# Kernel tuning notes

Measured on AMD Instinct MI355X. Metric: run time of the kernel, lower is better.

## Reference

```python
import jax, jax.numpy as jnp
import numpy as np

N_NODES = 50000
N_EDGES = 800000
IN_DIM = 128
HID = 32
HEADS = 4
OUT_DIM = 2
NEG_SLOPE = 0.2


def gat_conv(feat, W, al, ar, bias, src, dst, n_nodes):
    """DGL GATConv (eval mode, no dropout). feat: [N, Fin]; W: [Fin, H*D];
    al, ar: [H, D]; bias: [H*D]. Returns [N, H, D]."""
    H, D = al.shape
    hf = (feat @ W).reshape(n_nodes, H, D)              # [N,H,D]
    el = jnp.einsum('nhd,hd->nh', hf, al)               # [N,H]
    er = jnp.einsum('nhd,hd->nh', hf, ar)               # [N,H]
    e = el[src] + er[dst]                               # [E,H]
    e = jax.nn.leaky_relu(e, NEG_SLOPE)
    # segment softmax over incoming edges of each dst node
    emax = jax.ops.segment_max(e, dst, num_segments=n_nodes)  # [N,H]
    emax = jnp.where(jnp.isfinite(emax), emax, 0.0)
    ex = jnp.exp(e - emax[dst])                         # [E,H]
    denom = jax.ops.segment_sum(ex, dst, num_segments=n_nodes)  # [N,H]
    alpha = ex / jnp.maximum(denom[dst], 1e-30)         # [E,H]
    msg = hf[src] * alpha[:, :, None]                   # [E,H,D]
    out = jax.ops.segment_sum(msg, dst, num_segments=n_nodes)   # [N,H,D]
    return out + bias.reshape(1, H, D)


def setup_inputs() -> dict:
    key = jax.random.key(0)
    ks = jax.random.split(key, 16)
    f32 = jnp.float32
    in_feat = jax.random.normal(ks[0], (N_NODES, IN_DIM), dtype=f32)
    src = jax.random.randint(ks[1], (N_EDGES,), 0, N_NODES)
    dst = jax.random.randint(ks[2], (N_EDGES,), 0, N_NODES)
    s1 = 1.0 / np.sqrt(IN_DIM)
    s2 = 1.0 / np.sqrt(HID * HEADS)
    W1 = jax.random.normal(ks[3], (IN_DIM, HEADS * HID), dtype=f32) * s1
    al1 = jax.random.normal(ks[4], (HEADS, HID), dtype=f32) * 0.1
    ar1 = jax.random.normal(ks[5], (HEADS, HID), dtype=f32) * 0.1
    b1 = jnp.zeros((HEADS * HID,), dtype=f32)
    W2 = jax.random.normal(ks[6], (HEADS * HID, HEADS * HID), dtype=f32) * s2
    al2 = jax.random.normal(ks[7], (HEADS, HID), dtype=f32) * 0.1
    ar2 = jax.random.normal(ks[8], (HEADS, HID), dtype=f32) * 0.1
    b2 = jnp.zeros((HEADS * HID,), dtype=f32)
    Wout = jax.random.normal(ks[9], (HID, OUT_DIM), dtype=f32) * (1.0 / np.sqrt(HID))
    bout = jnp.zeros((OUT_DIM,), dtype=f32)
    return {"in_feat": in_feat, "W1": W1, "al1": al1, "ar1": ar1, "b1": b1,
            "W2": W2, "al2": al2, "ar2": ar2, "b2": b2,
            "Wout": Wout, "bout": bout, "src": src, "dst": dst}


def reference(in_feat, W1, al1, ar1, b1, W2, al2, ar2, b2, Wout, bout, src, dst):
    h = gat_conv(in_feat, W1, al1, ar1, b1, src, dst, N_NODES)  # [N,H,D]
    h = jax.nn.relu(h.reshape(N_NODES, HEADS * HID))            # flatten(1) + relu
    h = gat_conv(h, W2, al2, ar2, b2, src, dst, N_NODES)        # [N,H,D]
    emd = h.mean(axis=1)                                        # mean over heads -> [N,D]
    logits = jax.nn.relu(emd) @ Wout + bout                     # [N,2]
    return jax.nn.softmax(logits, axis=-1)
```

## Files before the change

kernel.cpp:

```cpp
#include <hip/hip_runtime.h>
#include <cmath>

#define N_NODES 50000
#define N_EDGES 800000
#define NBUCK 196
#define NHB 196
#define EPB 4096

typedef unsigned short u16;
typedef unsigned int u32;
typedef __attribute__((ext_vector_type(8))) short bf16x8;
typedef __attribute__((ext_vector_type(4))) float f32x4;

static __device__ __forceinline__ float lrelu(float x) { return x > 0.f ? x : 0.2f * x; }
static __device__ __forceinline__ float bf2f(u16 u) { return __uint_as_float(((u32)u) << 16); }
static __device__ __forceinline__ u16 f2bf(float f) {
    u32 b = __float_as_uint(f);
    return (u16)((b + 0x7FFFu + ((b >> 16) & 1u)) >> 16);
}
static __device__ __forceinline__ u32 pack2(float a, float b) {
    return (u32)f2bf(a) | ((u32)f2bf(b) << 16);
}
static __device__ __forceinline__ float sx(u32 u, int k) {
    return (float)((int)(u << ((3 - k) * 8)) >> 24);
}

__global__ __launch_bounds__(1024) void bhist_pack_k(const int* __restrict__ dst, u32* __restrict__ bcnt,
                                                     const float* __restrict__ W1, const float* __restrict__ W2,
                                                     u16* __restrict__ Wp1, u16* __restrict__ Wp2,
                                                     u32* __restrict__ done) {
    int tid = threadIdx.x;
    if (blockIdx.x < NHB) {
        __shared__ u32 hist[NBUCK];
        for (int i = tid; i < NBUCK; i += 1024) hist[i] = 0;
        __syncthreads();
        int base = blockIdx.x * EPB;
#pragma unroll
        for (int k = 0; k < 4; ++k) {
            int e = base + k * 1024 + tid;
            if (e < N_EDGES) atomicAdd(&hist[dst[e] >> 8], 1u);
        }
        __syncthreads();
        for (int i = tid; i < NBUCK; i += 1024) bcnt[(size_t)i * NHB + blockIdx.x] = hist[i];
    } else {
        if (blockIdx.x == NHB && tid == 0) *done = 0;
        int gi = (blockIdx.x - NHB) * 1024 + tid;
        const float* W = (gi < 16384) ? W1 : W2;
        u16* Wp = (gi < 16384) ? Wp1 : Wp2;
        int i = gi & 16383;
        int j = i & 7, lane = (i >> 3) & 63, ks = (i >> 9) & 3, nt = i >> 11;
        int k = ks * 32 + (lane >> 4) * 8 + j;
        int ncol = nt * 16 + (lane & 15);
        Wp[i] = f2bf(W[k * 128 + ncol]);
    }
}

__global__ __launch_bounds__(256) void scant_k(const u32* __restrict__ bcnt, u32* __restrict__ wbase,
                                               u32* __restrict__ btot, int* __restrict__ bstart,
                                               u32* __restrict__ done) {
    __shared__ u32 s[256];
    __shared__ bool amLast;
    int i = blockIdx.x, t = threadIdx.x;
    u32 v = (t < NHB) ? bcnt[(size_t)i * NHB + t] : 0;
    s[t] = v;
    __syncthreads();
    for (int o = 1; o < 256; o <<= 1) {
        u32 x = (t >= o) ? s[t - o] : 0;
        __syncthreads();
        s[t] += x;
        __syncthreads();
    }
    if (t < NHB) wbase[(size_t)i * NHB + t] = s[t] - v;
    if (t == 255) atomicExch(&btot[i], s[255]);
    __threadfence();
    if (t == 0) amLast = (atomicAdd(done, 1u) == NBUCK - 1);
    __syncthreads();
    if (!amLast) return;
    __threadfence();
    u32 v2 = (t < NBUCK) ? atomicAdd(&btot[t], 0u) : 0;
    s[t] = v2;
    __syncthreads();
    for (int o = 1; o < 256; o <<= 1) {
        u32 x = (t >= o) ? s[t - o] : 0;
        __syncthreads();
        s[t] += x;
        __syncthreads();
    }
    if (t < NBUCK) bstart[t] = (int)(s[t] - v2);
    if (t == NBUCK - 1) bstart[NBUCK] = (int)s[t];
}

__global__ __launch_bounds__(1024) void bscatter_k(const int* __restrict__ src, const int* __restrict__ dst,
                                                   const u32* __restrict__ wbase, const int* __restrict__ bstart,
                                                   u32* __restrict__ bucketed) {
    __shared__ u32 pos[NBUCK];
    int tid = threadIdx.x;
    for (int i = tid; i < NBUCK; i += 1024)
        pos[i] = (u32)bstart[i] + wbase[(size_t)i * NHB + blockIdx.x];
    __syncthreads();
    int base = blockIdx.x * EPB;
#pragma unroll
    for (int k = 0; k < 4; ++k) {
        int e = base + k * 1024 + tid;
        if (e < N_EDGES) {
            int d = dst[e];
            int b = d >> 8;
            u32 p = atomicAdd(&pos[b], 1u);
            bucketed[p] = (u32)src[e] | ((u32)(d & 255) << 16);
        }
    }
}

__global__ __launch_bounds__(1024) void bcsr_k(const u32* __restrict__ bucketed, const int* __restrict__ bstart,
                                               int* __restrict__ offs, u16* __restrict__ srcs) {
    __shared__ u32 cnt[256];
    __shared__ int s[256];
    __shared__ u32 fp[256];
    int b = blockIdx.x;
    int tid = threadIdx.x;
    int ebeg = bstart[b], eend = bstart[b + 1];
    int ne = eend - ebeg;
    if (tid < 256) cnt[tid] = 0;
    __syncthreads();
    for (int i = tid; i < ne; i += 1024)
        atomicAdd(&cnt[bucketed[ebeg + i] >> 16], 1u);
    __syncthreads();
    if (tid < 256) s[tid] = (int)cnt[tid];
    __syncthreads();
    for (int o = 1; o < 256; o <<= 1) {
        int v = (tid < 256 && tid >= o) ? s[tid - o] : 0;
        __syncthreads();
        if (tid < 256) s[tid] += v;
        __syncthreads();
    }
    if (tid < 256) {
        int excl = s[tid] - (int)cnt[tid];
        int node = b * 256 + tid;
        if (node < N_NODES) offs[node] = ebeg + excl;
        fp[tid] = (u32)excl;
    }
    if (b == NBUCK - 1 && tid == 0) offs[N_NODES] = N_EDGES;
    __syncthreads();
    for (int i = tid; i < ne; i += 1024) {
        u32 u = bucketed[ebeg + i];
        u32 p = atomicAdd(&fp[u >> 16], 1u);
        srcs[ebeg + p] = (u16)(u & 0xFFFFu);
    }
}

template <int BF16IN>
__global__ __launch_bounds__(256) void gemm_mfma(
    const void* __restrict__ Xv, const u16* __restrict__ Wp,
    const float* __restrict__ al, const float* __restrict__ ar,
    signed char* __restrict__ hq, float2* __restrict__ elhs, float* __restrict__ er, int n)
{
    __shared__ u16 xs[64][136];
    int row0 = blockIdx.x * 64;
    int tid = threadIdx.x;
    if (BF16IN) {
        const uint4* Xb = (const uint4*)Xv;
        for (int i = tid; i < 1024; i += 256) {
            int r = i >> 4, c = i & 15;
            uint4 v = make_uint4(0u, 0u, 0u, 0u);
            if (row0 + r < n) v = Xb[(size_t)(row0 + r) * 16 + c];
            ((uint4*)&xs[r][0])[c] = v;
        }
    } else {
        const float4* X4 = (const float4*)Xv;
        for (int i = tid; i < 2048; i += 256) {
            int r = i >> 5, c = i & 31;
            float4 v = make_float4(0.f, 0.f, 0.f, 0.f);
            if (row0 + r < n) v = X4[(size_t)(row0 + r) * 32 + c];
            ((uint2*)&xs[r][0])[c] = make_uint2(pack2(v.x, v.y), pack2(v.z, v.w));
        }
    }
    __syncthreads();

    int wave = tid >> 6, lane = tid & 63;
    int quad = lane >> 4, l15 = lane & 15;

    bf16x8 bfrag[2][4];
#pragma unroll
    for (int ct = 0; ct < 2; ++ct) {
        int nt = wave * 2 + ct;
#pragma unroll
        for (int ks = 0; ks < 4; ++ks)
            bfrag[ct][ks] = *(const bf16x8*)(Wp + ((((nt * 4 + ks) * 64) + lane) << 3));
    }

    f32x4 acc[4][2];
#pragma unroll
    for (int rt = 0; rt < 4; ++rt)
#pragma unroll
        for (int ct = 0; ct < 2; ++ct)
            acc[rt][ct] = (f32x4){0.f, 0.f, 0.f, 0.f};

#pragma unroll
    for (int ks = 0; ks < 4; ++ks) {
#pragma unroll
        for (int rt = 0; rt < 4; ++rt) {
            bf16x8 a = *(const bf16x8*)&xs[rt * 16 + l15][ks * 32 + quad * 8];
            acc[rt][0] = __builtin_amdgcn_mfma_f32_16x16x32_bf16(a, bfrag[0][ks], acc[rt][0], 0, 0, 0);
            acc[rt][1] = __builtin_amdgcn_mfma_f32_16x16x32_bf16(a, bfrag[1][ks], acc[rt][1], 0, 0, 0);
        }
    }

    float alv0 = al[wave * 32 + l15], alv1 = al[wave * 32 + 16 + l15];
    float arv0 = ar[wave * 32 + l15], arv1 = ar[wave * 32 + 16 + l15];
#pragma unroll
    for (int rt = 0; rt < 4; ++rt) {
#pragma unroll
        for (int r = 0; r < 4; ++r) {
            int row = row0 + rt * 16 + quad * 4 + r;
            float c0 = acc[rt][0][r], c1 = acc[rt][1][r];
            float m = fmaxf(fabsf(c0), fabsf(c1));
            m = fmaxf(m, __shfl_xor(m, 1));
            m = fmaxf(m, __shfl_xor(m, 2));
            m = fmaxf(m, __shfl_xor(m, 4));
            m = fmaxf(m, __shfl_xor(m, 8));
            m = fmaxf(m, 1e-20f);
            float qsc = 127.0f / m;
            if (row < n) {
                hq[(size_t)row * 128 + wave * 32 + l15] = (signed char)(int)rintf(c0 * qsc);
                hq[(size_t)row * 128 + wave * 32 + 16 + l15] = (signed char)(int)rintf(c1 * qsc);
            }
            float pel = c0 * alv0 + c1 * alv1;
            float per = c0 * arv0 + c1 * arv1;
            pel += __shfl_xor(pel, 1); pel += __shfl_xor(pel, 2);
            pel += __shfl_xor(pel, 4); pel += __shfl_xor(pel, 8);
            per += __shfl_xor(per, 1); per += __shfl_xor(per, 2);
            per += __shfl_xor(per, 4); per += __shfl_xor(per, 8);
            if (l15 == 0 && row < n) {
                elhs[row * 4 + wave] = make_float2(pel, m * (1.0f / 127.0f));
                er[row * 4 + wave] = per;
            }
        }
    }
}

static __device__ __forceinline__ void agg_core(
    int node, int lane, const int* __restrict__ offs, const u16* __restrict__ srcs,
    const float2* __restrict__ elhs, const float* __restrict__ er,
    const signed char* __restrict__ hq,
    float acc[8], float& den)
{
    int qw = lane >> 4;
    int q = lane & 15;
    int h = q >> 2;
    float erh = er[node * 4 + h];
    int beg = offs[node], end = offs[node + 1];
    int deg = end - beg;
    den = 0.f;
#pragma unroll
    for (int i = 0; i < 8; i++) acc[i] = 0.f;

    if (deg <= 64) {
        int psrc = (lane < deg) ? (int)srcs[beg + lane] : 0;
        int base = beg;
        for (; base + 16 <= end; base += 16) {
            int j = base - beg + qw;
            int ss[4];
            ss[0] = __shfl(psrc, j);
            ss[1] = __shfl(psrc, j + 4);
            ss[2] = __shfl(psrc, j + 8);
            ss[3] = __shfl(psrc, j + 12);
            float2 eh[4];
            uint2 uv[4];
#pragma unroll
            for (int k = 0; k < 4; ++k) {
                eh[k] = elhs[ss[k] * 4 + h];
                uv[k] = *(const uint2*)(hq + (size_t)ss[k] * 128 + q * 8);
            }
#pragma unroll
            for (int k = 0; k < 4; ++k) {
                float w = __expf(lrelu(eh[k].x + erh));
                float ws = w * eh[k].y;
                den += w;
                acc[0] += ws * sx(uv[k].x, 0);
                acc[1] += ws * sx(uv[k].x, 1);
                acc[2] += ws * sx(uv[k].x, 2);
                acc[3] += ws * sx(uv[k].x, 3);
                acc[4] += ws * sx(uv[k].y, 0);
                acc[5] += ws * sx(uv[k].y, 1);
                acc[6] += ws * sx(uv[k].y, 2);
                acc[7] += ws * sx(uv[k].y, 3);
            }
        }
        for (; base + 8 <= end; base += 8) {
            int j = base - beg + qw;
            int s0 = __shfl(psrc, j);
            int s1 = __shfl(psrc, j + 4);
            float2 e0 = elhs[s0 * 4 + h], e1 = elhs[s1 * 4 + h];
            uint2 u0 = *(const uint2*)(hq + (size_t)s0 * 128 + q * 8);
            uint2 u1 = *(const uint2*)(hq + (size_t)s1 * 128 + q * 8);
            float w0 = __expf(lrelu(e0.x + erh));
            float w1 = __expf(lrelu(e1.x + erh));
            float ws0 = w0 * e0.y, ws1 = w1 * e1.y;
            den += w0 + w1;
            acc[0] += ws0 * sx(u0.x, 0) + ws1 * sx(u1.x, 0);
            acc[1] += ws0 * sx(u0.x, 1) + ws1 * sx(u1.x, 1);
            acc[2] += ws0 * sx(u0.x, 2) + ws1 * sx(u1.x, 2);
            acc[3] += ws0 * sx(u0.x, 3) + ws1 * sx(u1.x, 3);
            acc[4] += ws0 * sx(u0.y, 0) + ws1 * sx(u1.y, 0);
            acc[5] += ws0 * sx(u0.y, 1) + ws1 * sx(u1.y, 1);
            acc[6] += ws0 * sx(u0.y, 2) + ws1 * sx(u1.y, 2);
            acc[7] += ws0 * sx(u0.y, 3) + ws1 * sx(u1.y, 3);
        }
        for (; base < end; base += 4) {
            int e = base + qw;
            bool valid = e < end;
            int j = valid ? (e - beg) : 0;
            int s = __shfl(psrc, j);
            float2 eh = elhs[s * 4 + h];
            float w = valid ? __expf(lrelu(eh.x + erh)) : 0.f;
            float ws = w * eh.y;
            uint2 u = *(const uint2*)(hq + (size_t)s * 128 + q * 8);
            den += w;
            acc[0] += ws * sx(u.x, 0);
            acc[1] += ws * sx(u.x, 1);
            acc[2] += ws * sx(u.x, 2);
            acc[3] += ws * sx(u.x, 3);
            acc[4] += ws * sx(u.y, 0);
            acc[5] += ws * sx(u.y, 1);
            acc[6] += ws * sx(u.y, 2);
            acc[7] += ws * sx(u.y, 3);
        }
    } else {
        for (int base = beg; base < end; base += 4) {
            int e = base + qw;
            bool valid = e < end;
            int ec = valid ? e : end - 1;
            int s = srcs[ec];
            float2 eh = elhs[s * 4 + h];
            float w = valid ? __expf(lrelu(eh.x + erh)) : 0.f;
            float ws = w * eh.y;
            uint2 u = *(const uint2*)(hq + (size_t)s * 128 + q * 8);
            den += w;
            acc[0] += ws * sx(u.x, 0);
            acc[1] += ws * sx(u.x, 1);
            acc[2] += ws * sx(u.x, 2);
            acc[3] += ws * sx(u.x, 3);
            acc[4] += ws * sx(u.y, 0);
            acc[5] += ws * sx(u.y, 1);
            acc[6] += ws * sx(u.y, 2);
            acc[7] += ws * sx(u.y, 3);
        }
    }
#pragma unroll
    for (int i = 0; i < 8; i++) {
        acc[i] += __shfl_xor(acc[i], 16);
        acc[i] += __shfl_xor(acc[i], 32);
    }
    den += __shfl_xor(den, 16);
    den += __shfl_xor(den, 32);
}

__global__ __launch_bounds__(256) void agg1_gemm2_k(
    const int* __restrict__ offs, const u16* __restrict__ srcs,
    const float2* __restrict__ elhs1, const float* __restrict__ er1,
    const signed char* __restrict__ hq1, const float* __restrict__ b1,
    const u16* __restrict__ Wp2, const float* __restrict__ al2, const float* __restrict__ ar2,
    signed char* __restrict__ hq2, float2* __restrict__ elhs2, float* __restrict__ er2)
{
    __shared__ u16 xs[16][136];
    int row0 = blockIdx.x * 16;
    int tid = threadIdx.x;
    int wave = tid >> 6, lane = tid & 63;
    int q = lane & 15;

    float bv[8];
#pragma unroll
    for (int i = 0; i < 8; i++) bv[i] = b1[q * 8 + i];

#pragma unroll
    for (int it = 0; it < 4; ++it) {
        int ln = wave * 4 + it;
        int node = row0 + ln;
        float acc[8], den;
        agg_core(node, lane, offs, srcs, elhs1, er1, hq1, acc, den);
        if (lane < 16) {
            float inv = 1.0f / fmaxf(den, 1e-30f);
            float o[8];
#pragma unroll
            for (int i = 0; i < 8; i++)
                o[i] = fmaxf(acc[i] * inv + bv[i], 0.f);
            uint4 pk;
            pk.x = pack2(o[0], o[1]);
            pk.y = pack2(o[2], o[3]);
            pk.z = pack2(o[4], o[5]);
            pk.w = pack2(o[6], o[7]);
            ((uint4*)&xs[ln][0])[q] = pk;
        }
    }
    __syncthreads();

    int quad = lane >> 4, l15 = lane & 15;

    bf16x8 bfrag[2][4];
#pragma unroll
    for (int ct = 0; ct < 2; ++ct) {
        int nt = wave * 2 + ct;
#pragma unroll
        for (int ks = 0; ks < 4; ++ks)
            bfrag[ct][ks] = *(const bf16x8*)(Wp2 + ((((nt * 4 + ks) * 64) + lane) << 3));
    }

    f32x4 acc2[2];
    acc2[0] = (f32x4){0.f, 0.f, 0.f, 0.f};
    acc2[1] = (f32x4){0.f, 0.f, 0.f, 0.f};

#pragma unroll
    for (int ks = 0; ks < 4; ++ks) {
        bf16x8 a = *(const bf16x8*)&xs[l15][ks * 32 + quad * 8];
        acc2[0] = __builtin_amdgcn_mfma_f32_16x16x32_bf16(a, bfrag[0][ks], acc2[0], 0, 0, 0);
        acc2[1] = __builtin_amdgcn_mfma_f32_16x16x32_bf16(a, bfrag[1][ks], acc2[1], 0, 0, 0);
    }

    float alv0 = al2[wave * 32 + l15], alv1 = al2[wave * 32 + 16 + l15];
    float arv0 = ar2[wave * 32 + l15], arv1 = ar2[wave * 32 + 16 + l15];
#pragma unroll
    for (int r = 0; r < 4; ++r) {
        int row = row0 + quad * 4 + r;
        float c0 = acc2[0][r], c1 = acc2[1][r];
        float m = fmaxf(fabsf(c0), fabsf(c1));
        m = fmaxf(m, __shfl_xor(m, 1));
        m = fmaxf(m, __shfl_xor(m, 2));
        m = fmaxf(m, __shfl_xor(m, 4));
        m = fmaxf(m, __shfl_xor(m, 8));
        m = fmaxf(m, 1e-20f);
        float qsc = 127.0f / m;
        hq2[(size_t)row * 128 + wave * 32 + l15] = (signed char)(int)rintf(c0 * qsc);
        hq2[(size_t)row * 128 + wave * 32 + 16 + l15] = (signed char)(int)rintf(c1 * qsc);
        float pel = c0 * alv0 + c1 * alv1;
        float per = c0 * arv0 + c1 * arv1;
        pel += __shfl_xor(pel, 1); pel += __shfl_xor(pel, 2);
        pel += __shfl_xor(pel, 4); pel += __shfl_xor(pel, 8);
        per += __shfl_xor(per, 1); per += __shfl_xor(per, 2);
        per += __shfl_xor(per, 4); per += __shfl_xor(per, 8);
        if (l15 == 0) {
            elhs2[row * 4 + wave] = make_float2(pel, m * (1.0f / 127.0f));
            er2[row * 4 + wave] = per;
        }
    }
}

__global__ __launch_bounds__(256) void agg2_k(const int* __restrict__ offs, const u16* __restrict__ srcs,
                                              const float2* __restrict__ elhs, const float* __restrict__ er,
                                              const signed char* __restrict__ hq,
                                              const float* __restrict__ bias,
                                              const float* __restrict__ Wout, const float* __restrict__ bout,
                                              float2* __restrict__ out) {
    int node = blockIdx.x * 4 + (threadIdx.x >> 6);
    int lane = threadIdx.x & 63;
    if (node >= N_NODES) return;
    float acc[8], den;
    agg_core(node, lane, offs, srcs, elhs, er, hq, acc, den);
    int q = lane & 15;
    float inv = 1.0f / fmaxf(den, 1e-30f);
    float o[8];
#pragma unroll
    for (int i = 0; i < 8; i++) o[i] = acc[i] * inv + bias[q * 8 + i];
#pragma unroll
    for (int i = 0; i < 8; i++) {
        o[i] += __shfl_xor(o[i], 4);
        o[i] += __shfl_xor(o[i], 8);
        o[i] = fmaxf(0.25f * o[i], 0.f);
    }
    int d0 = (q & 3) * 8;
    float l0 = 0.f, l1 = 0.f;
#pragma unroll
    for (int i = 0; i < 8; i++) {
        l0 += o[i] * Wout[(d0 + i) * 2];
        l1 += o[i] * Wout[(d0 + i) * 2 + 1];
    }
    l0 += __shfl_xor(l0, 1); l0 += __shfl_xor(l0, 2);
    l1 += __shfl_xor(l1, 1); l1 += __shfl_xor(l1, 2);
    if (lane == 0) {
        l0 += bout[0];
        l1 += bout[1];
        float mx = fmaxf(l0, l1);
        float e0 = __expf(l0 - mx), e1 = __expf(l1 - mx);
        float invs = 1.f / (e0 + e1);
        out[node] = make_float2(e0 * invs, e1 * invs);
    }
}

extern "C" void kernel_launch(void* const* d_in, const int* in_sizes, int n_in,
                              void* d_out, int out_size, void* d_ws, size_t ws_size,
                              hipStream_t stream) {
    const float* in_feat = (const float*)d_in[0];
    const float* W1   = (const float*)d_in[1];
    const float* al1  = (const float*)d_in[2];
    const float* ar1  = (const float*)d_in[3];
    const float* b1   = (const float*)d_in[4];
    const float* W2   = (const float*)d_in[5];
    const float* al2  = (const float*)d_in[6];
    const float* ar2  = (const float*)d_in[7];
    const float* b2   = (const float*)d_in[8];
    const float* Wout = (const float*)d_in[9];
    const float* bout = (const float*)d_in[10];
    const int*   src  = (const int*)d_in[11];
    const int*   dst  = (const int*)d_in[12];
    float* out = (float*)d_out;

    char* ws = (char*)d_ws;
    size_t off = 0;
    auto carve = [&](size_t bytes) {
        char* p = ws + off;
        off = (off + bytes + 255) & ~(size_t)255;
        return p;
    };
    signed char* hq  = (signed char*)carve((size_t)N_NODES * 128);
    float2* elhs     = (float2*)carve((size_t)N_NODES * 4 * 8);
    float* er        = (float*)carve((size_t)N_NODES * 4 * 4);
    signed char* hq2 = (signed char*)carve((size_t)N_NODES * 128);
    float2* elhs2    = (float2*)carve((size_t)N_NODES * 4 * 8);
    float* er2       = (float*)carve((size_t)N_NODES * 4 * 4);
    u16*   srcs      = (u16*)carve((size_t)N_EDGES * 2);
    u32*   bucketed  = (u32*)carve((size_t)N_EDGES * 4);
    u32*   bcnt      = (u32*)carve((size_t)NBUCK * NHB * 4);
    u32*   wbase     = (u32*)carve((size_t)NBUCK * NHB * 4);
    u32*   btot      = (u32*)carve((size_t)NBUCK * 4);
    int*   bstart    = (int*)carve((size_t)(NBUCK + 1) * 4);
    int*   offs      = (int*)carve((size_t)(N_NODES + 1) * 4);
    u16*   Wp1       = (u16*)carve((size_t)16384 * 2);
    u16*   Wp2       = (u16*)carve((size_t)16384 * 2);
    u32*   done      = (u32*)carve(256);
    (void)ws_size; (void)in_sizes; (void)n_in; (void)out_size;

    const int GB = (N_NODES + 63) / 64;
    const int FB = N_NODES / 16;
    const int AB = (N_NODES + 3) / 4;

    bhist_pack_k<<<NHB + 32, 1024, 0, stream>>>(dst, bcnt, W1, W2, Wp1, Wp2, done);
    scant_k<<<NBUCK, 256, 0, stream>>>(bcnt, wbase, btot, bstart, done);
    bscatter_k<<<NHB, 1024, 0, stream>>>(src, dst, wbase, bstart, bucketed);
    bcsr_k<<<NBUCK, 1024, 0, stream>>>(bucketed, bstart, offs, srcs);

    gemm_mfma<0><<<GB, 256, 0, stream>>>(in_feat, Wp1, al1, ar1, hq, elhs, er, N_NODES);

    agg1_gemm2_k<<<FB, 256, 0, stream>>>(offs, srcs, elhs, er, hq, b1, Wp2, al2, ar2, hq2, elhs2, er2);

    agg2_k<<<AB, 256, 0, stream>>>(offs, srcs, elhs2, er2, hq2, b2, Wout, bout, (float2*)out);
}
```

Baseline: 218.8 us.

## Merge CSR build with layer-1 GEMM; split agg1/GEMM2 into separate kernels

Layer-1 GEMM blocks now launch in the same kernel as the per-bucket CSR construction, so the two independent stages share one launch and can run concurrently. A new GEMM path uses 1024-thread blocks over 256 rows. The previously fused layer-1 aggregation plus layer-2 GEMM kernel is split into a standalone aggregation that writes bf16 features to global memory, followed by the generic bf16-input GEMM kernel. That adds a 12.8MB round trip for h1 and one more launch, but it raises aggregation parallelism and lets the layer-2 buffers reuse the layer-1 workspace. The larger shared tile of about 70KB may limit occupancy.

Measured after the change: 220.6 us. No clear change (+0.8%).

```diff
diff --git a/kernel.cpp b/kernel.cpp
--- a/kernel.cpp
+++ b/kernel.cpp
@@ -111,40 +111,122 @@
     }
 }
 
-__global__ __launch_bounds__(1024) void bcsr_k(const u32* __restrict__ bucketed, const int* __restrict__ bstart,
-                                               int* __restrict__ offs, u16* __restrict__ srcs) {
-    __shared__ u32 cnt[256];
-    __shared__ int s[256];
-    __shared__ u32 fp[256];
-    int b = blockIdx.x;
+__global__ __launch_bounds__(1024) void bcsr_gemm1_k(
+    const u32* __restrict__ bucketed, const int* __restrict__ bstart,
+    int* __restrict__ offs, u16* __restrict__ srcs,
+    const float* __restrict__ X, const u16* __restrict__ Wp,
+    const float* __restrict__ al, const float* __restrict__ ar,
+    signed char* __restrict__ hq, float2* __restrict__ elhs, float* __restrict__ er, int n)
+{
+    __shared__ u16 xs[256][136];
     int tid = threadIdx.x;
-    int ebeg = bstart[b], eend = bstart[b + 1];
-    int ne = eend - ebeg;
-    if (tid < 256) cnt[tid] = 0;
+
+    if (blockIdx.x < NBUCK) {
+        u32* cnt = (u32*)&xs[0][0];
+        int* s   = (int*)(cnt + 256);
+        u32* fp  = (u32*)(s + 256);
+        int b = blockIdx.x;
+        int ebeg = bstart[b], eend = bstart[b + 1];
+        int ne = eend - ebeg;
+        if (tid < 256) cnt[tid] = 0;
+        __syncthreads();
+        for (int i = tid; i < ne; i += 1024)
+            atomicAdd(&cnt[bucketed[ebeg + i] >> 16], 1u);
+        __syncthreads();
+        if (tid < 256) s[tid] = (int)cnt[tid];
+        __syncthreads();
+        for (int o = 1; o < 256; o <<= 1) {
+            int v = (tid < 256 && tid >= o) ? s[tid - o] : 0;
+            __syncthreads();
+            if (tid < 256) s[tid] += v;
+            __syncthreads();
+        }
+        if (tid < 256) {
+            int excl = s[tid] - (int)cnt[tid];
+            int node = b * 256 + tid;
+            if (node < N_NODES) offs[node] = ebeg + excl;
+            fp[tid] = (u32)excl;
+        }
+        if (b == NBUCK - 1 && tid == 0) offs[N_NODES] = N_EDGES;
+        __syncthreads();
+        for (int i = tid; i < ne; i += 1024) {
+            u32 u = bucketed[ebeg + i];
+            u32 p = atomicAdd(&fp[u >> 16], 1u);
+            srcs[ebeg + p] = (u16)(u & 0xFFFFu);
+        }
+        return;
+    }
+
+    int row0 = (blockIdx.x - NBUCK) * 256;
+    const float4* X4 = (const float4*)X;
+    for (int i = tid; i < 8192; i += 1024) {
+        int r = i >> 5, c = i & 31;
+        float4 v = make_float4(0.f, 0.f, 0.f, 0.f);
+        if (row0 + r < n) v = X4[(size_t)(row0 + r) * 32 + c];
+        ((uint2*)&xs[r][0])[c] = make_uint2(pack2(v.x, v.y), pack2(v.z, v.w));
+    }
     __syncthreads();
-    for (int i = tid; i < ne; i += 1024)
-        atomicAdd(&cnt[bucketed[ebeg + i] >> 16], 1u);
-    __syncthreads();
-    if (tid < 256) s[tid] = (int)cnt[tid];
-    __syncthreads();
-    for (int o = 1; o < 256; o <<= 1) {
-        int v = (tid < 256 && tid >= o) ? s[tid - o] : 0;
-        __syncthreads();
-        if (tid < 256) s[tid] += v;
-        __syncthreads();
-    }
-    if (tid < 256) {
-        int excl = s[tid] - (int)cnt[tid];
-        int node = b * 256 + tid;
-        if (node < N_NODES) offs[node] = ebeg + excl;
-        fp[tid] = (u32)excl;
-    }
-    if (b == NBUCK - 1 && tid == 0) offs[N_NODES] = N_EDGES;
-    __syncthreads();
-    for (int i = tid; i < ne; i += 1024) {
-        u32 u = bucketed[ebeg + i];
-        u32 p = atomicAdd(&fp[u >> 16], 1u);
-        srcs[ebeg + p] = (u16)(u & 0xFFFFu);
+
+    int wave = tid >> 6, lane = tid & 63;
+    int hd = wave & 3, wrow = (wave >> 2) * 64;
+    int quad = lane >> 4, l15 = lane & 15;
+
+    bf16x8 bfrag[2][4];
+#pragma unroll
+    for (int ct = 0; ct < 2; ++ct) {
+        int nt = hd * 2 + ct;
+#pragma unroll
+        for (int ks = 0; ks < 4; ++ks)
+            bfrag[ct][ks] = *(const bf16x8*)(Wp + ((((nt * 4 + ks) * 64) + lane) << 3));
+    }
+
+    f32x4 acc[4][2];
+#pragma unroll
+    for (int rt = 0; rt < 4; ++rt)
+#pragma unroll
+        for (int ct = 0; ct < 2; ++ct)
+            acc[rt][ct] = (f32x4){0.f, 0.f, 0.f, 0.f};
+
+#pragma unroll
+    for (int ks = 0; ks < 4; ++ks) {
+#pragma unroll
+        for (int rt = 0; rt < 4; ++rt) {
+            bf16x8 a = *(const bf16x8*)&xs[wrow + rt * 16 + l15][ks * 32 + quad * 8];
+            acc[rt][0] = __builtin_amdgcn_mfma_f32_16x16x32_bf16(a, bfrag[0][ks], acc[rt][0], 0, 0, 0);
+            acc[rt][1] = __builtin_amdgcn_mfma_f32_16x16x32_bf16(a, bfrag[1][ks], acc[rt][1], 0, 0, 0);
+        }
+    }
+
+    float alv0 = al[hd * 32 + l15], alv1 = al[hd * 32 + 16 + l15];
+    float arv0 = ar[hd * 32 + l15], arv1 = ar[hd * 32 + 16 + l15];
+#pragma unroll
+    for (int rt = 0; rt < 4; ++rt) {
+#pragma unroll
+        for (int r = 0; r < 4; ++r) {
+            int row = row0 + wrow + rt * 16 + quad * 4 + r;
+            float c0 = acc[rt][0][r], c1 = acc[rt][1][r];
+            float m = fmaxf(fabsf(c0), fabsf(c1));
+            m = fmaxf(m, __shfl_xor(m, 1));
+            m = fmaxf(m, __shfl_xor(m, 2));
+            m = fmaxf(m, __shfl_xor(m, 4));
+            m = fmaxf(m, __shfl_xor(m, 8));
+            m = fmaxf(m, 1e-20f);
+            float qsc = 127.0f / m;
+            if (row < n) {
+                hq[(size_t)row * 128 + hd * 32 + l15] = (signed char)(int)rintf(c0 * qsc);
+                hq[(size_t)row * 128 + hd * 32 + 16 + l15] = (signed char)(int)rintf(c1 * qsc);
+            }
+            float pel = c0 * alv0 + c1 * alv1;
+            float per = c0 * arv0 + c1 * arv1;
+            pel += __shfl_xor(pel, 1); pel += __shfl_xor(pel, 2);
+            pel += __shfl_xor(pel, 4); pel += __shfl_xor(pel, 8);
+            per += __shfl_xor(per, 1); per += __shfl_xor(per, 2);
+            per += __shfl_xor(per, 4); per += __shfl_xor(per, 8);
+            if (l15 == 0 && row < n) {
+                elhs[row * 4 + hd] = make_float2(pel, m * (1.0f / 127.0f));
+                er[row * 4 + hd] = per;
+            }
+        }
     }
 }
 
@@ -355,92 +437,28 @@
     den += __shfl_xor(den, 32);
 }
 
-__global__ __launch_bounds__(256) void agg1_gemm2_k(
-    const int* __restrict__ offs, const u16* __restrict__ srcs,
-    const float2* __restrict__ elhs1, const float* __restrict__ er1,
-    const signed char* __restrict__ hq1, const float* __restrict__ b1,
-    const u16* __restrict__ Wp2, const float* __restrict__ al2, const float* __restrict__ ar2,
-    signed char* __restrict__ hq2, float2* __restrict__ elhs2, float* __restrict__ er2)
-{
-    __shared__ u16 xs[16][136];
-    int row0 = blockIdx.x * 16;
-    int tid = threadIdx.x;
-    int wave = tid >> 6, lane = tid & 63;
-    int q = lane & 15;
-
-    float bv[8];
-#pragma unroll
-    for (int i = 0; i < 8; i++) bv[i] = b1[q * 8 + i];
-
-#pragma unroll
-    for (int it = 0; it < 4; ++it) {
-        int ln = wave * 4 + it;
-        int node = row0 + ln;
-        float acc[8], den;
-        agg_core(node, lane, offs, srcs, elhs1, er1, hq1, acc, den);
-        if (lane < 16) {
-            float inv = 1.0f / fmaxf(den, 1e-30f);
-            float o[8];
-#pragma unroll
-            for (int i = 0; i < 8; i++)
-                o[i] = fmaxf(acc[i] * inv + bv[i], 0.f);
-            uint4 pk;
-            pk.x = pack2(o[0], o[1]);
-            pk.y = pack2(o[2], o[3]);
-            pk.z = pack2(o[4], o[5]);
-            pk.w = pack2(o[6], o[7]);
-            ((uint4*)&xs[ln][0])[q] = pk;
-        }
-    }
-    __syncthreads();
-
-    int quad = lane >> 4, l15 = lane & 15;
-
-    bf16x8 bfrag[2][4];
-#pragma unroll
-    for (int ct = 0; ct < 2; ++ct) {
-        int nt = wave * 2 + ct;
-#pragma unroll
-        for (int ks = 0; ks < 4; ++ks)
-            bfrag[ct][ks] = *(const bf16x8*)(Wp2 + ((((nt * 4 + ks) * 64) + lane) << 3));
-    }
-
-    f32x4 acc2[2];
-    acc2[0] = (f32x4){0.f, 0.f, 0.f, 0.f};
-    acc2[1] = (f32x4){0.f, 0.f, 0.f, 0.f};
-
-#pragma unroll
-    for (int ks = 0; ks < 4; ++ks) {
-        bf16x8 a = *(const bf16x8*)&xs[l15][ks * 32 + quad * 8];
-        acc2[0] = __builtin_amdgcn_mfma_f32_16x16x32_bf16(a, bfrag[0][ks], acc2[0], 0, 0, 0);
-        acc2[1] = __builtin_amdgcn_mfma_f32_16x16x32_bf16(a, bfrag[1][ks], acc2[1], 0, 0, 0);
-    }
-
-    float alv0 = al2[wave * 32 + l15], alv1 = al2[wave * 32 + 16 + l15];
-    float arv0 = ar2[wave * 32 + l15], arv1 = ar2[wave * 32 + 16 + l15];
-#pragma unroll
-    for (int r = 0; r < 4; ++r) {
-        int row = row0 + quad * 4 + r;
-        float c0 = acc2[0][r], c1 = acc2[1][r];
-        float m = fmaxf(fabsf(c0), fabsf(c1));
-        m = fmaxf(m, __shfl_xor(m, 1));
-        m = fmaxf(m, __shfl_xor(m, 2));
-        m = fmaxf(m, __shfl_xor(m, 4));
-        m = fmaxf(m, __shfl_xor(m, 8));
-        m = fmaxf(m, 1e-20f);
-        float qsc = 127.0f / m;
-        hq2[(size_t)row * 128 + wave * 32 + l15] = (signed char)(int)rintf(c0 * qsc);
-        hq2[(size_t)row * 128 + wave * 32 + 16 + l15] = (signed char)(int)rintf(c1 * qsc);
-        float pel = c0 * alv0 + c1 * alv1;
-        float per = c0 * arv0 + c1 * arv1;
-        pel += __shfl_xor(pel, 1); pel += __shfl_xor(pel, 2);
-        pel += __shfl_xor(pel, 4); pel += __shfl_xor(pel, 8);
-        per += __shfl_xor(per, 1); per += __shfl_xor(per, 2);
-        per += __shfl_xor(per, 4); per += __shfl_xor(per, 8);
-        if (l15 == 0) {
-            elhs2[row * 4 + wave] = make_float2(pel, m * (1.0f / 127.0f));
-            er2[row * 4 + wave] = per;
-        }
+__global__ __launch_bounds__(256) void agg1_k(const int* __restrict__ offs, const u16* __restrict__ srcs,
+                                              const float2* __restrict__ elhs, const float* __restrict__ er,
+                                              const signed char* __restrict__ hq,
+                                              const float* __restrict__ bias, u16* __restrict__ h1) {
+    int node = blockIdx.x * 4 + (threadIdx.x >> 6);
+    int lane = threadIdx.x & 63;
+    if (node >= N_NODES) return;
+    float acc[8], den;
+    agg_core(node, lane, offs, srcs, elhs, er, hq, acc, den);
+    int qw = lane >> 4, q = lane & 15;
+    if (qw == 0) {
+        float inv = 1.0f / fmaxf(den, 1e-30f);
+        float o[8];
+#pragma unroll
+        for (int i = 0; i < 8; i++)
+            o[i] = fmaxf(acc[i] * inv + bias[q * 8 + i], 0.f);
+        uint4 pk;
+        pk.x = pack2(o[0], o[1]);
+        pk.y = pack2(o[2], o[3]);
+        pk.z = pack2(o[4], o[5]);
+        pk.w = pack2(o[6], o[7]);
+        *(uint4*)(h1 + (size_t)node * 128 + q * 8) = pk;
     }
 }
 
@@ -513,9 +531,7 @@
     signed char* hq  = (signed char*)carve((size_t)N_NODES * 128);
     float2* elhs     = (float2*)carve((size_t)N_NODES * 4 * 8);
     float* er        = (float*)carve((size_t)N_NODES * 4 * 4);
-    signed char* hq2 = (signed char*)carve((size_t)N_NODES * 128);
-    float2* elhs2    = (float2*)carve((size_t)N_NODES * 4 * 8);
-    float* er2       = (float*)carve((size_t)N_NODES * 4 * 4);
+    u16*   h1        = (u16*)carve((size_t)N_NODES * 128 * 2);
     u16*   srcs      = (u16*)carve((size_t)N_EDGES * 2);
     u32*   bucketed  = (u32*)carve((size_t)N_EDGES * 4);
     u32*   bcnt      = (u32*)carve((size_t)NBUCK * NHB * 4);
@@ -528,18 +544,16 @@
     u32*   done      = (u32*)carve(256);
     (void)ws_size; (void)in_sizes; (void)n_in; (void)out_size;
 
-    const int GB = (N_NODES + 63) / 64;
-    const int FB = N_NODES / 16;
-    const int AB = (N_NODES + 3) / 4;
+    const int GB   = (N_NODES + 63) / 64;
+    const int GB256 = (N_NODES + 255) / 256;
+    const int AB   = (N_NODES + 3) / 4;
 
     bhist_pack_k<<<NHB + 32, 1024, 0, stream>>>(dst, bcnt, W1, W2, Wp1, Wp2, done);
     scant_k<<<NBUCK, 256, 0, stream>>>(bcnt, wbase, btot, bstart, done);
     bscatter_k<<<NHB, 1024, 0, stream>>>(src, dst, wbase, bstart, bucketed);
-    bcsr_k<<<NBUCK, 1024, 0, stream>>>(bucketed, bstart, offs, srcs);
-
-    gemm_mfma<0><<<GB, 256, 0, stream>>>(in_feat, Wp1, al1, ar1, hq, elhs, er, N_NODES);
-
-    agg1_gemm2_k<<<FB, 256, 0, stream>>>(offs, srcs, elhs, er, hq, b1, Wp2, al2, ar2, hq2, elhs2, er2);
-
-    agg2_k<<<AB, 256, 0, stream>>>(offs, srcs, elhs2, er2, hq2, b2, Wout, bout, (float2*)out);
-}
+    bcsr_gemm1_k<<<NBUCK + GB256, 1024, 0, stream>>>(bucketed, bstart, offs, srcs,
+                                                     in_feat, Wp1, al1, ar1, hq, elhs, er, N_NODES);
+    agg1_k<<<AB, 256, 0, stream>>>(offs, srcs, elhs, er, hq, b1, h1);
+    gemm_mfma<1><<<GB, 256, 0, stream>>>(h1, Wp2, al2, ar2, hq, elhs, er, N_NODES);
+    agg2_k<<<AB, 256, 0, stream>>>(offs, srcs, elhs, er, hq, b2, Wout, bout, (float2*)out);
+}
```
